# Kernel optimization log

Hardware: AMD Instinct MI355X
Metric: run time of the kernel (lower is better)

Reference implementation:

```python
import jax, jax.numpy as jnp
import numpy as np

V = 32000      # vocab_size
CTX = 1024     # context_length
D = 768        # n_embd
H = 12         # n_heads
HD = D // H    # head_dim
L = 6          # n_layers
DFF = 4 * D
B, S = 2, 1024
EPS = 1e-5


def _layernorm(x, w, b):
    mu = jnp.mean(x, axis=-1, keepdims=True)
    var = jnp.mean(jnp.square(x - mu), axis=-1, keepdims=True)
    return (x - mu) * jax.lax.rsqrt(var + EPS) * w + b


def setup_inputs() -> dict:
    key = jax.random.key(0)
    ks = iter(jax.random.split(key, 32))
    s = 0.02
    idx = jax.random.randint(next(ks), (B, S), 0, V)
    p = {
        "idx": idx,
        "tok_emb": jax.random.normal(next(ks), (V, D), jnp.float32) * s,
        "pos_emb": jax.random.normal(next(ks), (CTX, D), jnp.float32) * s,
        "ln1_w": jnp.ones((L, D)), "ln1_b": jnp.zeros((L, D)),
        "Wq": jax.random.normal(next(ks), (L, D, D), jnp.float32) * s,
        "bq": jnp.zeros((L, D)),
        "Wk": jax.random.normal(next(ks), (L, D, D), jnp.float32) * s,
        "bk": jnp.zeros((L, D)),
        "Wv": jax.random.normal(next(ks), (L, D, D), jnp.float32) * s,
        "bv": jnp.zeros((L, D)),
        "Wo": jax.random.normal(next(ks), (L, D, D), jnp.float32) * s,
        "bo": jnp.zeros((L, D)),
        "ln2_w": jnp.ones((L, D)), "ln2_b": jnp.zeros((L, D)),
        "W1": jax.random.normal(next(ks), (L, D, DFF), jnp.float32) * s,
        "b1": jnp.zeros((L, DFF)),
        "W2": jax.random.normal(next(ks), (L, DFF, D), jnp.float32) * s,
        "b2": jnp.zeros((L, D)),
        "lnf_w": jnp.ones((D,)), "lnf_b": jnp.zeros((D,)),
        "lm_head_w": jax.random.normal(next(ks), (D, V), jnp.float32) * s,
    }
    return p


def _forward(idx, tok_emb, pos_emb, ln1_w, ln1_b, Wq, bq, Wk, bk, Wv, bv,
             Wo, bo, ln2_w, ln2_b, W1, b1, W2, b2, lnf_w, lnf_b, lm_head_w):
    b, s = idx.shape
    x = tok_emb[idx] + pos_emb[:s]  # [B,S,D]
    mask = jnp.tril(jnp.ones((s, s), dtype=bool))  # causal
    scale = 1.0 / np.sqrt(HD)
    for l in range(L):
        # --- attention ---
        h = _layernorm(x, ln1_w[l], ln1_b[l])
        q = (h @ Wq[l] + bq[l]).reshape(b, s, H, HD).transpose(0, 2, 1, 3)
        k = (h @ Wk[l] + bk[l]).reshape(b, s, H, HD).transpose(0, 2, 1, 3)
        v = (h @ Wv[l] + bv[l]).reshape(b, s, H, HD).transpose(0, 2, 1, 3)
        att = jnp.einsum('bhqd,bhkd->bhqk', q, k) * scale
        att = jnp.where(mask, att, -jnp.inf)
        att = jax.nn.softmax(att, axis=-1)
        y = jnp.einsum('bhqk,bhkd->bhqd', att, v)
        y = y.transpose(0, 2, 1, 3).reshape(b, s, D)
        x = x + y @ Wo[l] + bo[l]
        # --- MLP ---
        h2 = _layernorm(x, ln2_w[l], ln2_b[l])
        x = x + jax.nn.relu(h2 @ W1[l] + b1[l]) @ W2[l] + b2[l]
    logits = _layernorm(x, lnf_w, lnf_b) @ lm_head_w  # [B,S,V]
    return logits


def reference(idx, tok_emb, pos_emb, ln1_w, ln1_b, Wq, bq, Wk, bk, Wv, bv,
              Wo, bo, ln2_w, ln2_b, W1, b1, W2, b2, lnf_w, lnf_b, lm_head_w):
    return _forward(idx, tok_emb, pos_emb, ln1_w, ln1_b, Wq, bq, Wk, bk, Wv,
                    bv, Wo, bo, ln2_w, ln2_b, W1, b1, W2, b2, lnf_w, lnf_b,
                    lm_head_w)
```

## Files before the change

### kernel.cpp

```cpp
#include <hip/hip_runtime.h>
#include <hip/hip_bf16.h>
#include <math.h>

#define D 768
#define NH 12
#define HD 64
#define NL 6
#define DFF 3072
#define BB 2
#define SS 1024
#define NROWS (BB*SS)
#define VOCAB 32000
#define QKVN (3*D)
#define LN_EPS 1e-5f

typedef __attribute__((ext_vector_type(8))) short bf16x8;
typedef __attribute__((ext_vector_type(4))) float f32x4;

typedef __attribute__((address_space(1))) const unsigned char* gas_ptr;
typedef __attribute__((address_space(3))) unsigned char* las_ptr;

__device__ __forceinline__ void load_lds16(const void* g, void* l) {
    __builtin_amdgcn_global_load_lds((gas_ptr)g, (las_ptr)l, 16, 0, 0);
}

__device__ __forceinline__ void storeOut(float* p, float v) { *p = v; }
__device__ __forceinline__ void storeOut(__hip_bfloat16* p, float v) { *p = __float2bfloat16(v); }
__device__ __forceinline__ ushort f2bs(float f) {
    __hip_bfloat16 h = __float2bfloat16(f);
    return *(ushort*)&h;
}

#define WAIT_VMCNT(n) asm volatile("s_waitcnt vmcnt(" #n ")" ::: "memory")

__global__ void embed_kernel(const int* __restrict__ idx, const float* __restrict__ tok,
                             const float* __restrict__ pos, float* __restrict__ x) {
    int row = blockIdx.x;
    int s = row % SS;
    int t = idx[row];
    for (int c = threadIdx.x; c < D; c += blockDim.x)
        x[row*D + c] = tok[(size_t)t*D + c] + pos[s*D + c];
}

template<typename OT>
__global__ __launch_bounds__(256) void layernorm_kernel(const float* __restrict__ x,
                                                        const float* __restrict__ w,
                                                        const float* __restrict__ b,
                                                        OT* __restrict__ out) {
    int row = blockIdx.x;
    __shared__ float l1[4], l2[4];
    int base = row * D;
    float vals[3];
    float s1 = 0.f, s2 = 0.f;
#pragma unroll
    for (int i = 0; i < 3; i++) {
        float v = x[base + threadIdx.x + i*256];
        vals[i] = v; s1 += v; s2 += v*v;
    }
#pragma unroll
    for (int o = 32; o > 0; o >>= 1) {
        s1 += __shfl_down(s1, o, 64);
        s2 += __shfl_down(s2, o, 64);
    }
    if ((threadIdx.x & 63) == 0) { l1[threadIdx.x >> 6] = s1; l2[threadIdx.x >> 6] = s2; }
    __syncthreads();
    float sum   = l1[0] + l1[1] + l1[2] + l1[3];
    float sumsq = l2[0] + l2[1] + l2[2] + l2[3];
    float mu  = sum * (1.f / D);
    float var = sumsq * (1.f / D) - mu * mu;
    float inv = rsqrtf(var + LN_EPS);
#pragma unroll
    for (int i = 0; i < 3; i++) {
        int c = threadIdx.x + i*256;
        storeOut(&out[base + c], (vals[i] - mu) * inv * w[c] + b[c]);
    }
}

__global__ __launch_bounds__(256) void transpose_cvt(const float* __restrict__ src,
                                                     __hip_bfloat16* __restrict__ dst,
                                                     int K, int N,
                                                     size_t srcLayerStride, size_t dstLayerStride,
                                                     int dstRowOff) {
    int l = blockIdx.z;
    src += (size_t)l * srcLayerStride;
    dst += (size_t)l * dstLayerStride + (size_t)dstRowOff * K;
    __shared__ float t[32][33];
    int k0 = blockIdx.x*32, n0 = blockIdx.y*32;
    int tx = threadIdx.x & 31, ty = threadIdx.x >> 5;
    for (int i = ty; i < 32; i += 8) t[i][tx] = src[(size_t)(k0+i)*N + n0+tx];
    __syncthreads();
    for (int i = ty; i < 32; i += 8) dst[(size_t)(n0+i)*K + k0+tx] = __float2bfloat16(t[tx][i]);
}

__global__ __launch_bounds__(256) void qkvo_trans(const float* __restrict__ Wq,
                                                  const float* __restrict__ Wk,
                                                  const float* __restrict__ Wv,
                                                  const float* __restrict__ Wo,
                                                  __hip_bfloat16* __restrict__ qkvT,
                                                  __hip_bfloat16* __restrict__ WoT) {
    int z = blockIdx.z, l = z >> 2, m = z & 3;
    const float* src = (m==0 ? Wq : m==1 ? Wk : m==2 ? Wv : Wo) + (size_t)l*D*D;
    __hip_bfloat16* dst = (m < 3) ? qkvT + (size_t)l*QKVN*D + (size_t)m*D*D
                                  : WoT  + (size_t)l*D*D;
    __shared__ float t[32][33];
    int k0 = blockIdx.x*32, n0 = blockIdx.y*32;
    int tx = threadIdx.x & 31, ty = threadIdx.x >> 5;
    for (int i = ty; i < 32; i += 8) t[i][tx] = src[(size_t)(k0+i)*D + n0+tx];
    __syncthreads();
    for (int i = ty; i < 32; i += 8) dst[(size_t)(n0+i)*D + k0+tx] = __float2bfloat16(t[tx][i]);
}

__global__ void pack_qkv_bias(const float* __restrict__ bq, const float* __restrict__ bk,
                              const float* __restrict__ bv, float* __restrict__ dst) {
    int l = blockIdx.y;
    int i = blockIdx.x*256 + threadIdx.x;
    dst[l*QKVN + i]         = bq[l*D + i];
    dst[l*QKVN + D + i]     = bk[l*D + i];
    dst[l*QKVN + 2*D + i]   = bv[l*D + i];
}


#define GSTAGE(buf, k0) do {                                                     \
    _Pragma("unroll")                                                            \
    for (int i_ = 0; i_ < BM/64; i_++) {                                         \
        int rt_ = wid*(BM/4) + i_*16;                                            \
        load_lds16(A + (size_t)(bm + rt_ + lrow)*K + (k0) + lcol,                \
                   &As[buf][rt_][0]);                                            \
    }                                                                            \
    _Pragma("unroll")                                                            \
    for (int i_ = 0; i_ < BN/64; i_++) {                                         \
        int rt_ = wid*(BN/4) + i_*16;                                            \
        load_lds16(BT + (size_t)(bn + rt_ + lrow)*K + (k0) + lcol,               \
                   &Bs[buf][rt_][0]);                                            \
    } } while (0)

template<int BM, int BN, int CMAJ, typename OT, int RELU, int RESID, int HASB, int VSTORE>
__global__ __launch_bounds__(256) void gemm_mfma(const ushort* __restrict__ A,
                                                 const ushort* __restrict__ BT,
                                                 const float* __restrict__ bias,
                                                 const float* __restrict__ X,
                                                 OT* __restrict__ C,
                                                 ushort* __restrict__ vt,
                                                 int N, int K, int gx, int gy) {
    constexpr int WTM = BM/2, WTN = BN/2;
    constexpr int FRM = BM/32, FRN = BN/32;
    __shared__ ushort As[2][BM][32];
    __shared__ ushort Bs[2][BN][32];

    int id = blockIdx.x;
    int swz = (id & 7) * (gridDim.x >> 3) + (id >> 3);
    int bx, by;
    if (CMAJ) { bx = swz / gy; by = swz - bx * gy; }
    else      { by = swz / gx; bx = swz - by * gx; }
    int bm = by * BM, bn = bx * BN;

    int tid = threadIdx.x;
    int lane = tid & 63, wid = tid >> 6;
    int wr = wid >> 1, wc = wid & 1;
    int lrow = lane >> 2;
    int lcol = (((lane & 3) ^ ((lane >> 3) & 3)) * 8);
    int fr = lane & 15, fc = lane >> 4;
    int rchunk = (fc ^ ((fr >> 1) & 3)) * 8;

    f32x4 acc[FRM][FRN];
#pragma unroll
    for (int i = 0; i < FRM; i++)
#pragma unroll
        for (int j = 0; j < FRN; j++)
#pragma unroll
            for (int r = 0; r < 4; r++) acc[i][j][r] = 0.f;

    GSTAGE(0, 0);
    asm volatile("s_waitcnt vmcnt(0)" ::: "memory");
    __syncthreads();

    int cur = 0;
    for (int t = 0; t < K/32; t++) {
        if (t*32 + 32 < K) GSTAGE(cur^1, t*32 + 32);
        bf16x8 af[FRM], bf[FRN];
#pragma unroll
        for (int mi = 0; mi < FRM; mi++)
            af[mi] = *(const bf16x8*)&As[cur][wr*WTM + mi*16 + fr][rchunk];
#pragma unroll
        for (int ni = 0; ni < FRN; ni++)
            bf[ni] = *(const bf16x8*)&Bs[cur][wc*WTN + ni*16 + fr][rchunk];
        __builtin_amdgcn_s_setprio(1);
#pragma unroll
        for (int mi = 0; mi < FRM; mi++)
#pragma unroll
            for (int ni = 0; ni < FRN; ni++)
                acc[mi][ni] = __builtin_amdgcn_mfma_f32_16x16x32_bf16(af[mi], bf[ni], acc[mi][ni], 0, 0, 0);
        __builtin_amdgcn_s_setprio(0);
        asm volatile("s_waitcnt vmcnt(0)" ::: "memory");
        __syncthreads();
        cur ^= 1;
    }

    if (VSTORE && bn >= 2*D) {
        int hh = (bn - 2*D) / HD;
        int b  = bm >> 10;
        size_t vbase = ((size_t)(b*NH + hh)) * HD;
        int srow0 = (bm & (SS-1)) + wr*WTM + fc*4;
#pragma unroll
        for (int mi = 0; mi < FRM; mi++) {
#pragma unroll
            for (int ni = 0; ni < FRN; ni++) {
                int col = bn + wc*WTN + ni*16 + fr;
                int d   = wc*WTN + ni*16 + fr;
                float bv_ = bias[col];
                ushort4 u;
                u.x = f2bs(acc[mi][ni][0] + bv_);
                u.y = f2bs(acc[mi][ni][1] + bv_);
                u.z = f2bs(acc[mi][ni][2] + bv_);
                u.w = f2bs(acc[mi][ni][3] + bv_);
                *(ushort4*)&vt[(vbase + d)*SS + srow0 + mi*16] = u;
            }
        }
    } else {
#pragma unroll
        for (int mi = 0; mi < FRM; mi++) {
#pragma unroll
            for (int r = 0; r < 4; r++) {
                int row = bm + wr*WTM + mi*16 + fc*4 + r;
#pragma unroll
                for (int ni = 0; ni < FRN; ni++) {
                    int col = bn + wc*WTN + ni*16 + fr;
                    float v = acc[mi][ni][r];
                    if (HASB) v += bias[col];
                    if (RESID) v += X[(size_t)row * N + col];
                    if (RELU) v = fmaxf(v, 0.f);
                    storeOut(&C[(size_t)row * N + col], v);
                }
            }
        }
    }
}

#define RSTAGE(slot, k0) do {                                                    \
    int row_ = tid >> 2;                                                         \
    load_lds16(A  + (size_t)(bm + row_)*K + (k0) + sc_,                          \
               (char*)As + (size_t)(slot)*4096 + (size_t)wid*1024);              \
    load_lds16(BT + (size_t)(bn + row_)*K + (k0) + sc_,                          \
               (char*)Bs + (size_t)(slot)*4096 + (size_t)wid*1024);              \
    } while (0)

template<int RELU>
__global__ __launch_bounds__(256) void gemm_ring64(const ushort* __restrict__ A,
                                                   const ushort* __restrict__ BT,
                                                   const float* __restrict__ bias,
                                                   const float* __restrict__ X,
                                                   float* __restrict__ C,
                                                   int N, int K, int gx) {
    __shared__ ushort As[4][64][32];
    __shared__ ushort Bs[4][64][32];

    int id = blockIdx.x;
    int swz = (id & 7) * (gridDim.x >> 3) + (id >> 3);
    int by = swz / gx, bx = swz - by * gx;
    int bm = by * 64, bn = bx * 64;

    int tid = threadIdx.x;
    int lane = tid & 63, wid = tid >> 6;
    int wr = wid >> 1, wc = wid & 1;
    int sc_ = ((lane & 3) ^ ((lane >> 3) & 3)) * 8;
    int fr = lane & 15, fc = lane >> 4;
    int rchunk = (fc ^ ((fr >> 1) & 3)) * 8;

    f32x4 acc[2][2];
#pragma unroll
    for (int i = 0; i < 2; i++)
#pragma unroll
        for (int j = 0; j < 2; j++)
#pragma unroll
            for (int r = 0; r < 4; r++) acc[i][j][r] = 0.f;

    const int NT = K / 32;
    RSTAGE(0, 0);
    RSTAGE(1, 32);
    RSTAGE(2, 64);

    for (int t = 0; t < NT; t++) {
        if (t < NT-2)      WAIT_VMCNT(4);
        else if (t == NT-2) WAIT_VMCNT(2);
        else               WAIT_VMCNT(0);
        __builtin_amdgcn_s_barrier();
        asm volatile("" ::: "memory");
        if (t + 3 < NT) RSTAGE((t+3) & 3, (t+3)*32);
        int s = t & 3;
        bf16x8 af[2], bf[2];
#pragma unroll
        for (int mi = 0; mi < 2; mi++)
            af[mi] = *(const bf16x8*)&As[s][wr*32 + mi*16 + fr][rchunk];
#pragma unroll
        for (int ni = 0; ni < 2; ni++)
            bf[ni] = *(const bf16x8*)&Bs[s][wc*32 + ni*16 + fr][rchunk];
        __builtin_amdgcn_s_setprio(1);
#pragma unroll
        for (int mi = 0; mi < 2; mi++)
#pragma unroll
            for (int ni = 0; ni < 2; ni++)
                acc[mi][ni] = __builtin_amdgcn_mfma_f32_16x16x32_bf16(af[mi], bf[ni], acc[mi][ni], 0, 0, 0);
        __builtin_amdgcn_s_setprio(0);
    }

#pragma unroll
    for (int mi = 0; mi < 2; mi++) {
#pragma unroll
        for (int r = 0; r < 4; r++) {
            int row = bm + wr*32 + mi*16 + fc*4 + r;
#pragma unroll
            for (int ni = 0; ni < 2; ni++) {
                int col = bn + wc*32 + ni*16 + fr;
                float v = acc[mi][ni][r] + bias[col] + X[(size_t)row * N + col];
                if (RELU) v = fmaxf(v, 0.f);
                C[(size_t)row * N + col] = v;
            }
        }
    }
}

#define LMS(slot, k0) do {                                                        \
    _Pragma("unroll")                                                             \
    for (int i_ = 0; i_ < 2; i_++) {                                              \
        int row_ = i_*128 + (tid >> 2);                                           \
        size_t db_ = (size_t)(i_*512 + wid*64) * 16;                              \
        load_lds16(A  + (size_t)(bm + row_)*D + (k0) + sc_,                       \
                   (char*)As + (size_t)(slot)*16384 + db_);                       \
        load_lds16(BT + (size_t)(bn + row_)*D + (k0) + sc_,                       \
                   (char*)Bs + (size_t)(slot)*16384 + db_);                       \
    } } while (0)

__global__ __launch_bounds__(512) void lm256_gemm(const ushort* __restrict__ A,
                                                  const ushort* __restrict__ BT,
                                                  float* __restrict__ C) {
    constexpr int NT = D / 32;
    __shared__ ushort As[4][256][32];
    __shared__ ushort Bs[4][256][32];

    int id = blockIdx.x;
    int swz = (id & 7) * 125 + (id >> 3);
    int by = swz & 7;
    int bx = swz >> 3;
    int bm = by * 256, bn = bx * 256;

    int tid = threadIdx.x;
    int lane = tid & 63, wid = tid >> 6;
    int wr = wid >> 2, wc = wid & 3;
    int sc_ = ((tid & 3) ^ ((tid >> 3) & 3)) * 8;
    int fr = lane & 15, fc = lane >> 4;
    int rchunk = (fc ^ ((fr >> 1) & 3)) * 8;

    f32x4 acc[8][4];
#pragma unroll
    for (int i = 0; i < 8; i++)
#pragma unroll
        for (int j = 0; j < 4; j++)
#pragma unroll
            for (int r = 0; r < 4; r++) acc[i][j][r] = 0.f;

    LMS(0, 0);
    LMS(1, 32);
    LMS(2, 64);

    for (int t = 0; t < NT; t++) {
        if (t < NT-2)      WAIT_VMCNT(8);
        else if (t == NT-2) WAIT_VMCNT(4);
        else               WAIT_VMCNT(0);
        __builtin_amdgcn_s_barrier();
        asm volatile("" ::: "memory");
        if (t + 3 < NT) LMS((t+3) & 3, (t+3)*32);
        int s = t & 3;
        bf16x8 bfr[4];
#pragma unroll
        for (int ni = 0; ni < 4; ni++)
            bfr[ni] = *(const bf16x8*)&Bs[s][wc*64 + ni*16 + fr][rchunk];
        __builtin_amdgcn_s_setprio(1);
#pragma unroll
        for (int mi = 0; mi < 8; mi++) {
            bf16x8 a0 = *(const bf16x8*)&As[s][wr*128 + mi*16 + fr][rchunk];
#pragma unroll
            for (int ni = 0; ni < 4; ni++)
                acc[mi][ni] = __builtin_amdgcn_mfma_f32_16x16x32_bf16(a0, bfr[ni], acc[mi][ni], 0, 0, 0);
        }
        __builtin_amdgcn_s_setprio(0);
    }

#pragma unroll
    for (int mi = 0; mi < 8; mi++)
#pragma unroll
        for (int r = 0; r < 4; r++) {
            int row = bm + wr*128 + mi*16 + fc*4 + r;
            float* cp = C + (size_t)row * VOCAB + bn + wc*64 + fr;
#pragma unroll
            for (int ni = 0; ni < 4; ni++)
                cp[ni*16] = acc[mi][ni][r];
        }
}

#define KVSTAGE(buf, kv0) do {                                                   \
    _Pragma("unroll")                                                            \
    for (int j_ = 0; j_ < 2; j_++) {                                             \
        int r_ = w*16 + j_*8 + srow8;                                            \
        load_lds16(qkv + (size_t)(b*SS + (kv0) + r_)*QKVN + D + h*HD + schunk*8, \
                   &Ks[buf][w*16 + j_*8][0]);                                    \
        load_lds16(vt + ((size_t)(b*NH + h)*HD + r_)*SS + (kv0) + schunk*8,      \
                   &Vs[buf][w*16 + j_*8][0]);                                    \
    } } while (0)

__global__ __launch_bounds__(256) void attn_mfma(const ushort* __restrict__ qkv,
                                                 const ushort* __restrict__ vt,
                                                 __hip_bfloat16* __restrict__ y) {
    const int bx = blockIdx.x;
    const int qt = 15 - (bx & 15);
    const int h  = (bx >> 4) % NH;
    const int b  = bx / (16*NH);
    const int tid  = threadIdx.x;
    const int lane = tid & 63, w = tid >> 6;
    const int fr = lane & 15, fc = lane >> 4;

    __shared__ ushort Qs[64][64];
    __shared__ ushort Ks[2][64][64];
    __shared__ ushort Vs[2][64][64];
    __shared__ ushort Ps[4][16][72];

    const int q0 = qt * 64;
    const int srow8  = lane >> 3;
    const int schunk = (lane & 7) ^ srow8;

#pragma unroll
    for (int j = 0; j < 2; j++) {
        int r = w*16 + j*8 + srow8;
        load_lds16(qkv + (size_t)(b*SS + q0 + r)*QKVN + h*HD + schunk*8, &Qs[w*16 + j*8][0]);
    }
    KVSTAGE(0, 0);
    asm volatile("s_waitcnt vmcnt(0)" ::: "memory");
    __syncthreads();
    bf16x8 qf[2];
#pragma unroll
    for (int s = 0; s < 2; s++)
        qf[s] = *(const bf16x8*)&Qs[w*16 + fr][((s*4 + fc) ^ (fr & 7))*8];

    f32x4 oacc[4];
#pragma unroll
    for (int ni = 0; ni < 4; ni++)
#pragma unroll
        for (int r = 0; r < 4; r++) oacc[ni][r] = 0.f;
    float m[4] = {-INFINITY, -INFINITY, -INFINITY, -INFINITY};
    float l[4] = {0.f, 0.f, 0.f, 0.f};

    int cur = 0;
    for (int kt = 0; kt <= qt; kt++) {
        if (kt < qt) KVSTAGE(cur^1, (kt+1)*64);
        f32x4 sacc[4];
#pragma unroll
        for (int ni = 0; ni < 4; ni++)
#pragma unroll
            for (int r = 0; r < 4; r++) sacc[ni][r] = 0.f;
#pragma unroll
        for (int ni = 0; ni < 4; ni++)
#pragma unroll
            for (int s = 0; s < 2; s++) {
                bf16x8 kf = *(const bf16x8*)&Ks[cur][ni*16 + fr][((s*4 + fc) ^ (fr & 7))*8];
                sacc[ni] = __builtin_amdgcn_mfma_f32_16x16x32_bf16(qf[s], kf, sacc[ni], 0, 0, 0);
            }
        if (kt == qt) {
#pragma unroll
            for (int ni = 0; ni < 4; ni++)
#pragma unroll
                for (int r = 0; r < 4; r++) {
                    float v = sacc[ni][r] * 0.125f;
                    sacc[ni][r] = (ni*16 + fr > w*16 + fc*4 + r) ? -INFINITY : v;
                }
        } else {
#pragma unroll
            for (int ni = 0; ni < 4; ni++)
#pragma unroll
                for (int r = 0; r < 4; r++) sacc[ni][r] *= 0.125f;
        }
        float p[4][4];
#pragma unroll
        for (int r = 0; r < 4; r++) {
            float mx = fmaxf(fmaxf(sacc[0][r], sacc[1][r]), fmaxf(sacc[2][r], sacc[3][r]));
#pragma unroll
            for (int o = 1; o < 16; o <<= 1) mx = fmaxf(mx, __shfl_xor(mx, o, 64));
            float mn = fmaxf(m[r], mx);
            float fac = __expf(m[r] - mn);
            float rs = 0.f;
#pragma unroll
            for (int ni = 0; ni < 4; ni++) {
                float pv = __expf(sacc[ni][r] - mn);
                p[ni][r] = pv;
                rs += pv;
            }
#pragma unroll
            for (int o = 1; o < 16; o <<= 1) rs += __shfl_xor(rs, o, 64);
            l[r] = l[r] * fac + rs;
            m[r] = mn;
#pragma unroll
            for (int ni = 0; ni < 4; ni++) oacc[ni][r] *= fac;
        }
#pragma unroll
        for (int ni = 0; ni < 4; ni++)
#pragma unroll
            for (int r = 0; r < 4; r++)
                Ps[w][fc*4 + r][ni*16 + fr] = f2bs(p[ni][r]);
        bf16x8 pa[2];
#pragma unroll
        for (int s = 0; s < 2; s++) pa[s] = *(const bf16x8*)&Ps[w][fr][s*32 + fc*8];
#pragma unroll
        for (int ni = 0; ni < 4; ni++)
#pragma unroll
            for (int s = 0; s < 2; s++) {
                bf16x8 vf = *(const bf16x8*)&Vs[cur][ni*16 + fr][((s*4 + fc) ^ (fr & 7))*8];
                oacc[ni] = __builtin_amdgcn_mfma_f32_16x16x32_bf16(pa[s], vf, oacc[ni], 0, 0, 0);
            }
        asm volatile("s_waitcnt vmcnt(0)" ::: "memory");
        __syncthreads();
        cur ^= 1;
    }
#pragma unroll
    for (int r = 0; r < 4; r++) {
        float rinv = 1.f / l[r];
        int row = b*SS + q0 + w*16 + fc*4 + r;
#pragma unroll
        for (int ni = 0; ni < 4; ni++)
            y[(size_t)row*D + h*HD + ni*16 + fr] = __float2bfloat16(oacc[ni][r] * rinv);
    }
}

extern "C" void kernel_launch(void* const* d_in, const int* in_sizes, int n_in,
                              void* d_out, int out_size, void* d_ws, size_t ws_size,
                              hipStream_t stream) {
    const int*   idx  = (const int*)d_in[0];
    const float* tok  = (const float*)d_in[1];
    const float* pos  = (const float*)d_in[2];
    const float* ln1w = (const float*)d_in[3];
    const float* ln1b = (const float*)d_in[4];
    const float* Wq   = (const float*)d_in[5];
    const float* bq   = (const float*)d_in[6];
    const float* Wk   = (const float*)d_in[7];
    const float* bk   = (const float*)d_in[8];
    const float* Wv   = (const float*)d_in[9];
    const float* bv   = (const float*)d_in[10];
    const float* Wo   = (const float*)d_in[11];
    const float* bo   = (const float*)d_in[12];
    const float* ln2w = (const float*)d_in[13];
    const float* ln2b = (const float*)d_in[14];
    const float* W1   = (const float*)d_in[15];
    const float* b1   = (const float*)d_in[16];
    const float* W2   = (const float*)d_in[17];
    const float* b2   = (const float*)d_in[18];
    const float* lnfw = (const float*)d_in[19];
    const float* lnfb = (const float*)d_in[20];
    const float* lmw  = (const float*)d_in[21];
    float* out = (float*)d_out;

    char* p = (char*)d_ws;
    __hip_bfloat16* qkvT = (__hip_bfloat16*)p; p += (size_t)NL*QKVN*D*2;
    __hip_bfloat16* WoT  = (__hip_bfloat16*)p; p += (size_t)NL*D*D*2;
    __hip_bfloat16* W1T  = (__hip_bfloat16*)p; p += (size_t)NL*DFF*D*2;
    __hip_bfloat16* W2T  = (__hip_bfloat16*)p; p += (size_t)NL*D*DFF*2;
    __hip_bfloat16* lmT  = (__hip_bfloat16*)p; p += (size_t)VOCAB*D*2;
    float*          bqkv = (float*)p;          p += (size_t)NL*QKVN*4;
    float*          x    = (float*)p;          p += (size_t)NROWS*D*4;
    __hip_bfloat16* h    = (__hip_bfloat16*)p; p += (size_t)NROWS*D*2;
    __hip_bfloat16* qkv  = (__hip_bfloat16*)p; p += (size_t)NROWS*QKVN*2;
    __hip_bfloat16* vt   = (__hip_bfloat16*)p; p += (size_t)BB*NH*HD*SS*2;
    __hip_bfloat16* yb   = (__hip_bfloat16*)p; p += (size_t)NROWS*D*2;
    __hip_bfloat16* a1   = (__hip_bfloat16*)p; p += (size_t)NROWS*DFF*2;

    qkvo_trans<<<dim3(D/32, D/32, NL*4), 256, 0, stream>>>(Wq, Wk, Wv, Wo, qkvT, WoT);
    transpose_cvt<<<dim3(D/32, DFF/32, NL), 256, 0, stream>>>(W1, W1T, D, DFF, (size_t)D*DFF, (size_t)DFF*D, 0);
    transpose_cvt<<<dim3(DFF/32, D/32, NL), 256, 0, stream>>>(W2, W2T, DFF, D, (size_t)DFF*D, (size_t)D*DFF, 0);
    transpose_cvt<<<dim3(D/32, VOCAB/32, 1), 256, 0, stream>>>(lmw, lmT, D, VOCAB, 0, 0, 0);
    pack_qkv_bias<<<dim3(3, NL), 256, 0, stream>>>(bq, bk, bv, bqkv);

    embed_kernel<<<NROWS, 256, 0, stream>>>(idx, tok, pos, x);

    for (int l = 0; l < NL; l++) {
        layernorm_kernel<<<NROWS, 256, 0, stream>>>(x, ln1w + l*D, ln1b + l*D, h);
        gemm_mfma<128,64,0,__hip_bfloat16,0,0,1,1><<<576, 256, 0, stream>>>(
            (const ushort*)h, (const ushort*)(qkvT + (size_t)l*QKVN*D),
            bqkv + (size_t)l*QKVN, nullptr, qkv, (ushort*)vt, QKVN, D, QKVN/64, NROWS/128);
        attn_mfma<<<BB*NH*(SS/64), 256, 0, stream>>>((const ushort*)qkv, (const ushort*)vt, yb);
        gemm_ring64<0><<<384, 256, 0, stream>>>(
            (const ushort*)yb, (const ushort*)(WoT + (size_t)l*D*D),
            bo + (size_t)l*D, x, x, D, D, D/64);
        layernorm_kernel<<<NROWS, 256, 0, stream>>>(x, ln2w + l*D, ln2b + l*D, h);
        gemm_mfma<128,128,0,__hip_bfloat16,1,0,1,0><<<384, 256, 0, stream>>>(
            (const ushort*)h, (const ushort*)(W1T + (size_t)l*DFF*D),
            b1 + (size_t)l*DFF, nullptr, a1, nullptr, DFF, D, DFF/128, NROWS/128);
        gemm_ring64<0><<<384, 256, 0, stream>>>(
            (const ushort*)a1, (const ushort*)(W2T + (size_t)l*D*DFF),
            b2 + (size_t)l*D, x, x, D, DFF, D/64);
    }
    layernorm_kernel<<<NROWS, 256, 0, stream>>>(x, lnfw, lnfb, h);
    lm256_gemm<<<1000, 512, 0, stream>>>((const ushort*)h, (const ushort*)lmT, out);
}
```

Measured before the change: 1.232 ms.

## Restructure LM-head GEMM into 3-stage ping-pong pipeline with split A/B loads

Reworks the 256x256 LM-head GEMM main loop from a 4-slot prefetch ring into a 3-slot ring. Each K-step is split into two halves: the A-tile prefetch is issued before the first half of MFMAs and the B-tile prefetch before the second half, with barriers between halves. The aim is to interleave global-to-LDS traffic with MFMA work and cut LDS use so more blocks fit per CU. The cost is four barriers per K-step instead of one, and a shallower prefetch depth.

```diff
diff --git a/kernel.cpp b/kernel.cpp
--- a/kernel.cpp
+++ b/kernel.cpp
@@ -119,7 +119,6 @@
     dst[l*QKVN + 2*D + i]   = bv[l*D + i];
 }
 
-
 #define GSTAGE(buf, k0) do {                                                     \
     _Pragma("unroll")                                                            \
     for (int i_ = 0; i_ < BM/64; i_++) {                                         \
@@ -319,36 +318,40 @@
     }
 }
 
-#define LMS(slot, k0) do {                                                        \
+#define LMSA3(slot, k0) do {                                                      \
     _Pragma("unroll")                                                             \
     for (int i_ = 0; i_ < 2; i_++) {                                              \
         int row_ = i_*128 + (tid >> 2);                                           \
-        size_t db_ = (size_t)(i_*512 + wid*64) * 16;                              \
-        load_lds16(A  + (size_t)(bm + row_)*D + (k0) + sc_,                       \
-                   (char*)As + (size_t)(slot)*16384 + db_);                       \
-        load_lds16(BT + (size_t)(bn + row_)*D + (k0) + sc_,                       \
-                   (char*)Bs + (size_t)(slot)*16384 + db_);                       \
+        load_lds16(A + (size_t)(bm + row_)*D + (k0) + sc_,                        \
+                   (char*)As3 + (size_t)(slot)*16384 + (size_t)(i_*512 + wid*64)*16); \
+    } } while (0)
+#define LMSB3(slot, k0) do {                                                      \
+    _Pragma("unroll")                                                             \
+    for (int i_ = 0; i_ < 2; i_++) {                                              \
+        int row_ = i_*128 + (tid >> 2);                                           \
+        load_lds16(BT + (size_t)(bm_n + row_)*D + (k0) + sc_,                     \
+                   (char*)Bs3 + (size_t)(slot)*16384 + (size_t)(i_*512 + wid*64)*16); \
     } } while (0)
 
 __global__ __launch_bounds__(512) void lm256_gemm(const ushort* __restrict__ A,
                                                   const ushort* __restrict__ BT,
                                                   float* __restrict__ C) {
-    constexpr int NT = D / 32;
-    __shared__ ushort As[4][256][32];
-    __shared__ ushort Bs[4][256][32];
+    constexpr int NKT = D / 32;
+    __shared__ ushort As3[3][256][32];
+    __shared__ ushort Bs3[3][256][32];
 
     int id = blockIdx.x;
     int swz = (id & 7) * 125 + (id >> 3);
     int by = swz & 7;
     int bx = swz >> 3;
-    int bm = by * 256, bn = bx * 256;
+    int bm = by * 256, bm_n = bx * 256;
 
     int tid = threadIdx.x;
     int lane = tid & 63, wid = tid >> 6;
     int wr = wid >> 2, wc = wid & 3;
     int sc_ = ((tid & 3) ^ ((tid >> 3) & 3)) * 8;
     int fr = lane & 15, fc = lane >> 4;
-    int rchunk = (fc ^ ((fr >> 1) & 3)) * 8;
+    int rch = (fc ^ ((fr >> 1) & 3)) * 8;
 
     f32x4 acc[8][4];
 #pragma unroll
@@ -358,31 +361,47 @@
 #pragma unroll
             for (int r = 0; r < 4; r++) acc[i][j][r] = 0.f;
 
-    LMS(0, 0);
-    LMS(1, 32);
-    LMS(2, 64);
-
-    for (int t = 0; t < NT; t++) {
-        if (t < NT-2)      WAIT_VMCNT(8);
-        else if (t == NT-2) WAIT_VMCNT(4);
-        else               WAIT_VMCNT(0);
+    LMSA3(0, 0);  LMSB3(0, 0);
+    LMSA3(1, 32); LMSB3(1, 32);
+    WAIT_VMCNT(4);
+    __builtin_amdgcn_s_barrier();
+
+    int s = 0;
+    for (int j = 0; j < NKT; j++) {
+        int s2 = s + 2; if (s2 >= 3) s2 -= 3;
+        int kf2 = (j + 2) * 32;
+        bf16x8 bfr[4], af[4];
+#pragma unroll
+        for (int ni = 0; ni < 4; ni++)
+            bfr[ni] = *(const bf16x8*)&Bs3[s][wc*64 + ni*16 + fr][rch];
+#pragma unroll
+        for (int dm = 0; dm < 4; dm++)
+            af[dm] = *(const bf16x8*)&As3[s][wr*128 + dm*16 + fr][rch];
+        if (j + 2 < NKT) LMSA3(s2, kf2);
         __builtin_amdgcn_s_barrier();
-        asm volatile("" ::: "memory");
-        if (t + 3 < NT) LMS((t+3) & 3, (t+3)*32);
-        int s = t & 3;
-        bf16x8 bfr[4];
-#pragma unroll
-        for (int ni = 0; ni < 4; ni++)
-            bfr[ni] = *(const bf16x8*)&Bs[s][wc*64 + ni*16 + fr][rchunk];
         __builtin_amdgcn_s_setprio(1);
 #pragma unroll
-        for (int mi = 0; mi < 8; mi++) {
-            bf16x8 a0 = *(const bf16x8*)&As[s][wr*128 + mi*16 + fr][rchunk];
+        for (int dm = 0; dm < 4; dm++)
 #pragma unroll
             for (int ni = 0; ni < 4; ni++)
-                acc[mi][ni] = __builtin_amdgcn_mfma_f32_16x16x32_bf16(a0, bfr[ni], acc[mi][ni], 0, 0, 0);
-        }
+                acc[dm][ni] = __builtin_amdgcn_mfma_f32_16x16x32_bf16(af[dm], bfr[ni], acc[dm][ni], 0, 0, 0);
         __builtin_amdgcn_s_setprio(0);
+        __builtin_amdgcn_s_barrier();
+#pragma unroll
+        for (int dm = 0; dm < 4; dm++)
+            af[dm] = *(const bf16x8*)&As3[s][wr*128 + (4+dm)*16 + fr][rch];
+        if (j + 2 < NKT) { LMSB3(s2, kf2); WAIT_VMCNT(2); }
+        else             { WAIT_VMCNT(0); }
+        __builtin_amdgcn_s_barrier();
+        __builtin_amdgcn_s_setprio(1);
+#pragma unroll
+        for (int dm = 0; dm < 4; dm++)
+#pragma unroll
+            for (int ni = 0; ni < 4; ni++)
+                acc[4+dm][ni] = __builtin_amdgcn_mfma_f32_16x16x32_bf16(af[dm], bfr[ni], acc[4+dm][ni], 0, 0, 0);
+        __builtin_amdgcn_s_setprio(0);
+        __builtin_amdgcn_s_barrier();
+        s = s + 1; if (s >= 3) s = 0;
     }
 
 #pragma unroll
@@ -390,7 +409,7 @@
 #pragma unroll
         for (int r = 0; r < 4; r++) {
             int row = bm + wr*128 + mi*16 + fc*4 + r;
-            float* cp = C + (size_t)row * VOCAB + bn + wc*64 + fr;
+            float* cp = C + (size_t)row * VOCAB + bm_n + wc*64 + fr;
 #pragma unroll
             for (int ni = 0; ni < 4; ni++)
                 cp[ni*16] = acc[mi][ni][r];
```

After: 1.195 ms. 3.0% less time.
